# Kernel optimization log

Hardware: AMD Instinct MI355X
Metric: run time of the kernel (lower is better)

Reference implementation:

```python
import jax, jax.numpy as jnp
import numpy as np

EPS = 1e-12  # matches torch F.normalize default eps


def setup_inputs() -> dict:
    key = jax.random.key(0)
    k1, = jax.random.split(key, 1)
    N, M, D = 1024, 40, 768
    x = jax.random.normal(k1, (N, M, D), dtype=jnp.float32)
    w = jnp.asarray(15.0, dtype=jnp.float32)
    b = jnp.asarray(-7.0, dtype=jnp.float32)
    return {"x": x, "w": w, "b": b}


def reference(x, w, b):
    N, M, D = x.shape
    # L2 normalize along feature dim (torch F.normalize: x / max(||x||, eps))
    norm = jnp.linalg.norm(x, axis=-1, keepdims=True)
    xn = x / jnp.maximum(norm, EPS)
    # Inclusive centroids [N, D]
    c_incl = jnp.mean(xn, axis=1)
    # Exclusive centroids [N, M, D]: leave-one-out mean
    c_excl = (M * c_incl[:, None, :] - xn) / (M - 1)
    # Similarity of every utterance to every inclusive centroid: [N, M, N]
    sim = jnp.einsum('nmd,kd->nmk', xn, c_incl)
    # Own-speaker column uses the exclusive centroid instead (vectorized
    # replacement of the per-speaker diagonal-block loop)
    diag = jnp.sum(xn * c_excl, axis=-1)                 # [N, M]
    own = jnp.eye(N, dtype=bool)[:, None, :]             # [N, 1, N]
    sim = jnp.where(own, diag[:, :, None], sim)
    # Affine scale then cross-entropy against speaker labels
    logits = (w * sim + b).reshape(N * M, N)
    labels = jnp.repeat(jnp.arange(N), M)                # [N*M]
    lse = jax.nn.logsumexp(logits, axis=-1)
    picked = jnp.take_along_axis(logits, labels[:, None], axis=1)[:, 0]
    loss = jnp.mean(lse - picked)
    return loss
```

## Files before the change

kernel.cpp:

```cpp
#include <hip/hip_runtime.h>
#include <hip/hip_bf16.h>
#include <hip/hip_fp8.h>

typedef float f32x4 __attribute__((ext_vector_type(4)));
typedef long long i64;
typedef i64 i64x2 __attribute__((ext_vector_type(2)));

#define N_SPK 1024
#define M_UTT 40
#define D_FEAT 768
#define NROWS (N_SPK * M_UTT)
#define LOG2E 1.44269504088896340736f
#define LN2   0.69314718055994530942f

#define BM 128
#define BN 128
#define BKB 64
#define KT (D_FEAT / BKB)
#define ROWB 768

#define INV_SS (1.0f / 64.0f)
#define SCL 8.0f

__device__ __forceinline__ unsigned char to_fp8(float v) {
  __hip_fp8_e4m3 t(v);
  return (unsigned char)t.__x;
}

__device__ __forceinline__ int perm4base(int k0) {
  const int b = k0 & 63;
  return (k0 & ~63) + ((b >> 3) & 3) * 16 + (b & 7) + ((b >> 5) << 3);
}

__global__ __launch_bounds__(256) void k_norm_cent(const float* __restrict__ x,
                                                   unsigned char* __restrict__ xn,
                                                   unsigned char* __restrict__ cc) {
  const int n = blockIdx.x, t = threadIdx.x;
  const int lane = t & 63, wv = t >> 6;
  const float4* xb4 = (const float4*)(x + (size_t)n * (M_UTT * D_FEAT));
  unsigned char* ob = xn + (size_t)n * (M_UTT * D_FEAT);

  __shared__ float bins[2][4][3];
  __shared__ float cl[4][192][4];

  int o_[3], c4_[3], soff_[3];
#pragma unroll
  for (int q = 0; q < 3; ++q) {
    const int f = q * 256 + t;
    o_[q]  = f / 192;
    c4_[q] = f % 192;
    soff_[q] = perm4base(4 * c4_[q]);
  }

  float cacc[3][4];
#pragma unroll
  for (int q = 0; q < 3; ++q)
#pragma unroll
    for (int c = 0; c < 4; ++c) cacc[q][c] = 0.f;

  for (int g = 0; g < M_UTT / 4; ++g) {
    const int p = g & 1;
    float4 v[3];
#pragma unroll
    for (int q = 0; q < 3; ++q) v[q] = xb4[g * 768 + q * 256 + t];
    float ss[3];
#pragma unroll
    for (int q = 0; q < 3; ++q)
      ss[q] = v[q].x * v[q].x + v[q].y * v[q].y + v[q].z * v[q].z + v[q].w * v[q].w;
#pragma unroll
    for (int d = 1; d < 64; d <<= 1) {
      ss[0] += __shfl_xor(ss[0], d, 64);
      ss[1] += __shfl_xor(ss[1], d, 64);
      ss[2] += __shfl_xor(ss[2], d, 64);
    }
    if (lane == 0) {
#pragma unroll
      for (int q = 0; q < 3; ++q) {
        const int idx = 4 * q + wv;
        bins[p][idx / 3][idx % 3] = ss[q];
      }
    }
    __syncthreads();
#pragma unroll
    for (int q = 0; q < 3; ++q) {
      const int o = o_[q];
      const float tot = bins[p][o][0] + bins[p][o][1] + bins[p][o][2];
      const float iv = 1.0f / fmaxf(sqrtf(tot), 1e-12f);
      const float w0 = v[q].x * iv, w1 = v[q].y * iv, w2 = v[q].z * iv, w3 = v[q].w * iv;
      cacc[q][0] += w0; cacc[q][1] += w1; cacc[q][2] += w2; cacc[q][3] += w3;
      uchar4 u;
      u.x = to_fp8(w0 * SCL); u.y = to_fp8(w1 * SCL);
      u.z = to_fp8(w2 * SCL); u.w = to_fp8(w3 * SCL);
      *(uchar4*)(ob + (size_t)(4 * g + o) * D_FEAT + soff_[q]) = u;
    }
  }

#pragma unroll
  for (int q = 0; q < 3; ++q) {
#pragma unroll
    for (int c = 0; c < 4; ++c) cl[o_[q]][c4_[q]][c] = cacc[q][c];
  }
  __syncthreads();
  if (t < 192) {
    float s[4];
#pragma unroll
    for (int c = 0; c < 4; ++c)
      s[c] = cl[0][t][c] + cl[1][t][c] + cl[2][t][c] + cl[3][t][c];
    const float sc = SCL / (float)M_UTT;
    uchar4 u;
    u.x = to_fp8(s[0] * sc); u.y = to_fp8(s[1] * sc);
    u.z = to_fp8(s[2] * sc); u.w = to_fp8(s[3] * sc);
    *(uchar4*)(cc + (size_t)n * D_FEAT + perm4base(4 * t)) = u;
  }
}

#define GLD(g, l) __builtin_amdgcn_global_load_lds( \
    (const __attribute__((address_space(1))) unsigned int*)(g), \
    (__attribute__((address_space(3))) unsigned int*)(l), 16, 0, 0)

__global__ __launch_bounds__(256, 4) void k_gemm_part(
    const unsigned char* __restrict__ XN, const unsigned char* __restrict__ CC,
    const float* __restrict__ wp, const float* __restrict__ bp,
    float2* __restrict__ ppart, float* __restrict__ picked2) {

  __shared__ __align__(16) char smem[32768];

  const int tid  = threadIdx.x;
  const int wave = tid >> 6, lane = tid & 63;
  const int l16  = lane & 15, lg = lane >> 4;
  const int wr   = wave >> 1, wc = wave & 1;

  const int bid = blockIdx.x;
  const int xcd = bid & 7;
  const int tt  = bid >> 3;
  const int rb  = xcd * 40 + (tt >> 3);
  const int cb  = tt & 7;
  const int rowbase = rb * BM;
  const int colbase = cb * BN;

  const int R7   = (tid >> 3) & 7;
  const int li   = ((tid & 7) * 16) ^ (R7 << 4);
  const int row0 = 2 * (tid >> 3) + (li >> 6);
  const int kb   = li & 63;
  const int t16  = tid * 16;
  const unsigned char* gA = XN + (size_t)(rowbase + row0) * ROWB + kb;
  const unsigned char* gB = CC + (size_t)(colbase + row0) * ROWB + kb;

  const int xr  = ((l16 >> 1) & 7) << 4;
  const int in0 = ((((l16 & 1) << 6) | (lg << 4)) ^ xr);
  int aoff[4], boff[4];
#pragma unroll
  for (int i = 0; i < 4; ++i) {
    aoff[i] = (wr * 32 + i * 8 + (l16 >> 1)) * 128 + in0;
    boff[i] = 8192 + (wc * 32 + i * 8 + (l16 >> 1)) * 128 + in0;
  }

  f32x4 acc[4][4];
#pragma unroll
  for (int i = 0; i < 4; ++i)
#pragma unroll
    for (int jj = 0; jj < 4; ++jj) acc[i][jj] = (f32x4){0.f, 0.f, 0.f, 0.f};

  auto STAGE = [&](int buf, int koff) {
    char* sb = smem + buf * 16384;
    GLD(gA + koff,              sb + t16);
    GLD(gA + 64 * ROWB + koff,  sb + 4096 + t16);
    GLD(gB + koff,              sb + 8192 + t16);
    GLD(gB + 64 * ROWB + koff,  sb + 12288 + t16);
  };

  STAGE(0, 0);

  for (int k = 0; k < KT; ++k) {
    const char* bb = smem + (k & 1) * 16384;
    if (k + 1 < KT) {
      STAGE((k + 1) & 1, (k + 1) * BKB);
      asm volatile("s_waitcnt vmcnt(4)" ::: "memory");
    } else {
      asm volatile("s_waitcnt vmcnt(0)" ::: "memory");
    }
    __builtin_amdgcn_s_barrier();

    i64x2 av[4], bv[4];
#pragma unroll
    for (int i = 0; i < 4; ++i) av[i] = *(const i64x2*)(bb + aoff[i]);
#pragma unroll
    for (int jj = 0; jj < 4; ++jj) bv[jj] = *(const i64x2*)(bb + boff[jj]);
    __builtin_amdgcn_s_setprio(1);
#pragma unroll
    for (int i = 0; i < 4; ++i)
#pragma unroll
      for (int jj = 0; jj < 4; ++jj)
        acc[i][jj] = __builtin_amdgcn_mfma_f32_16x16x32_fp8_fp8(av[i][0], bv[jj][0], acc[i][jj], 0, 0, 0);
#pragma unroll
    for (int i = 0; i < 4; ++i)
#pragma unroll
      for (int jj = 0; jj < 4; ++jj)
        acc[i][jj] = __builtin_amdgcn_mfma_f32_16x16x32_fp8_fp8(av[i][1], bv[jj][1], acc[i][jj], 0, 0, 0);
    __builtin_amdgcn_s_setprio(0);
    asm volatile("s_waitcnt lgkmcnt(0)" ::: "memory");
    __builtin_amdgcn_s_barrier();
  }

  const float ws2 = wp[0] * LOG2E;
  const float b2  = bp[0] * LOG2E;
  float2* red = (float2*)smem;

#pragma unroll
  for (int i = 0; i < 4; ++i) {
#pragma unroll
    for (int rr = 0; rr < 4; ++rr) {
      const int lrow = wr * 64 + i * 16 + lg * 4 + rr;
      const int R = rowbase + lrow;
      const int n = R / M_UTT;
      float l2[4];
#pragma unroll
      for (int jj = 0; jj < 4; ++jj) {
        float sim = acc[i][jj][rr] * INV_SS;
        const int gc = colbase + wc * 64 + jj * 16 + l16;
        if (gc == n) {
          sim = (40.f * sim - 1.f) * (1.f / 39.f);
          picked2[R] = fmaf(ws2, sim, b2);
        }
        l2[jj] = fmaf(ws2, sim, b2);
      }
      float mx = fmaxf(fmaxf(l2[0], l2[1]), fmaxf(l2[2], l2[3]));
#pragma unroll
      for (int d = 1; d < 16; d <<= 1) mx = fmaxf(mx, __shfl_xor(mx, d, 64));
      float s = exp2f(l2[0] - mx) + exp2f(l2[1] - mx) +
                exp2f(l2[2] - mx) + exp2f(l2[3] - mx);
#pragma unroll
      for (int d = 1; d < 16; d <<= 1) s += __shfl_xor(s, d, 64);
      if (l16 == 0) red[lrow * 2 + wc] = make_float2(mx, s);
    }
  }
  __syncthreads();
  if (tid < 128) {
    const float2 p0 = red[tid * 2 + 0];
    const float2 p1 = red[tid * 2 + 1];
    const float m2 = fmaxf(p0.x, p1.x);
    const float ss = p0.y * exp2f(p0.x - m2) + p1.y * exp2f(p1.x - m2);
    ppart[(size_t)(rowbase + tid) * 8 + cb] = make_float2(m2, ss);
  }
}

__global__ __launch_bounds__(256) void k_combine(const float2* __restrict__ pp,
                                                 const float* __restrict__ picked2,
                                                 double* __restrict__ partial) {
  const int t = threadIdx.x;
  const int R = blockIdx.x * 256 + t;
  const float2* p = pp + (size_t)R * 8;
  float2 v[8];
#pragma unroll
  for (int j = 0; j < 8; ++j) v[j] = p[j];
  float m2 = v[0].x;
#pragma unroll
  for (int j = 1; j < 8; ++j) m2 = fmaxf(m2, v[j].x);
  float s = 0.f;
#pragma unroll
  for (int j = 0; j < 8; ++j) s += v[j].y * exp2f(v[j].x - m2);
  const float lse2 = m2 + log2f(s);
  const float rl = (lse2 - picked2[R]) * LN2;

  __shared__ double sm[256];
  sm[t] = (double)rl;
  __syncthreads();
  for (int off = 128; off > 0; off >>= 1) {
    if (t < off) sm[t] += sm[t + off];
    __syncthreads();
  }
  if (t == 0) partial[blockIdx.x] = sm[0];
}

__global__ __launch_bounds__(256) void k_reduce(const double* __restrict__ partial,
                                                float* __restrict__ out) {
  const int t = threadIdx.x;
  __shared__ double sm[256];
  sm[t] = (t < NROWS / 256) ? partial[t] : 0.0;
  __syncthreads();
  for (int off = 128; off > 0; off >>= 1) {
    if (t < off) sm[t] += sm[t + off];
    __syncthreads();
  }
  if (t == 0) out[0] = (float)(sm[0] / (double)NROWS);
}

extern "C" void kernel_launch(void* const* d_in, const int* in_sizes, int n_in,
                              void* d_out, int out_size, void* d_ws, size_t ws_size,
                              hipStream_t stream) {
  const float* x = (const float*)d_in[0];
  const float* w = (const float*)d_in[1];
  const float* b = (const float*)d_in[2];
  char* ws = (char*)d_ws;
  size_t off = 0;
  unsigned char* xn = (unsigned char*)(ws + off); off += (size_t)NROWS * D_FEAT;
  unsigned char* cc = (unsigned char*)(ws + off); off += (size_t)N_SPK * D_FEAT;
  off = (off + 255) & ~(size_t)255;
  float2* ppart   = (float2*)(ws + off); off += (size_t)NROWS * 8 * sizeof(float2);
  float* picked2  = (float*)(ws + off);  off += (size_t)NROWS * sizeof(float);
  off = (off + 255) & ~(size_t)255;
  double* partial = (double*)(ws + off); off += (size_t)(NROWS / 256) * sizeof(double);
  float* out = (float*)d_out;

  k_norm_cent<<<N_SPK, 256, 0, stream>>>(x, xn, cc);
  k_gemm_part<<<(NROWS / BM) * (N_SPK / BN), 256, 0, stream>>>(xn, cc, w, b, ppart, picked2);
  k_combine<<<NROWS / 256, 256, 0, stream>>>(ppart, picked2, partial);
  k_reduce<<<1, 256, 0, stream>>>(partial, out);
}
```

Before: 95.12 us.

## Enlarge GEMM row tile to 160 rows with a five-fragment MFMA loop

Raises the row tile of the fused similarity/logsumexp GEMM from 128 to 160. The grid becomes 2048 blocks, which gives a better wave count on the CUs and more reuse of each B tile across rows. A third async global-to-LDS load fills the extra 32 A rows, and threads that have nothing to load write into a dummy scratch region. The inner loop now loads each A fragment right before its MFMAs instead of preloading all of them. The cost is more accumulator registers (80) and more LDS per block, which may limit occupancy. The host launch must also change to match the new block count.

```diff
diff --git a/kernel.cpp b/kernel.cpp
--- a/kernel.cpp
+++ b/kernel.cpp
@@ -13,11 +13,15 @@
 #define LOG2E 1.44269504088896340736f
 #define LN2   0.69314718055994530942f
 
-#define BM 128
+#define BM 160
 #define BN 128
 #define BKB 64
 #define KT (D_FEAT / BKB)
 #define ROWB 768
+
+#define ABYTES 10240
+#define TILEB  18432
+#define SCRATCH 36864
 
 #define INV_SS (1.0f / 64.0f)
 #define SCL 8.0f
@@ -123,7 +127,7 @@
     const float* __restrict__ wp, const float* __restrict__ bp,
     float2* __restrict__ ppart, float* __restrict__ picked2) {
 
-  __shared__ __align__(16) char smem[32768];
+  __shared__ __align__(16) char smem[38912];
 
   const int tid  = threadIdx.x;
   const int wave = tid >> 6, lane = tid & 63;
@@ -132,71 +136,74 @@
 
   const int bid = blockIdx.x;
   const int xcd = bid & 7;
-  const int tt  = bid >> 3;
-  const int rb  = xcd * 40 + (tt >> 3);
-  const int cb  = tt & 7;
+  const int idx = bid >> 3;
+  const int rb  = xcd * 32 + (idx >> 3);
+  const int cb  = idx & 7;
   const int rowbase = rb * BM;
   const int colbase = cb * BN;
 
-  const int R7   = (tid >> 3) & 7;
-  const int li   = ((tid & 7) * 16) ^ (R7 << 4);
+  const int li   = ((tid & 7) * 16) ^ (((tid >> 3) & 7) << 4);
   const int row0 = 2 * (tid >> 3) + (li >> 6);
   const int kb   = li & 63;
   const int t16  = tid * 16;
   const unsigned char* gA = XN + (size_t)(rowbase + row0) * ROWB + kb;
   const unsigned char* gB = CC + (size_t)(colbase + row0) * ROWB + kb;
+  char* c2dst = (tid < 128) ? (char*)nullptr : nullptr;
 
   const int xr  = ((l16 >> 1) & 7) << 4;
   const int in0 = ((((l16 & 1) << 6) | (lg << 4)) ^ xr);
-  int aoff[4], boff[4];
-#pragma unroll
-  for (int i = 0; i < 4; ++i) {
-    aoff[i] = (wr * 32 + i * 8 + (l16 >> 1)) * 128 + in0;
-    boff[i] = 8192 + (wc * 32 + i * 8 + (l16 >> 1)) * 128 + in0;
-  }
-
-  f32x4 acc[4][4];
-#pragma unroll
-  for (int i = 0; i < 4; ++i)
+  int aoff[5], boff[4];
+#pragma unroll
+  for (int i = 0; i < 5; ++i)
+    aoff[i] = (wr * 40 + i * 8 + (l16 >> 1)) * 128 + in0;
+#pragma unroll
+  for (int jj = 0; jj < 4; ++jj)
+    boff[jj] = ABYTES + (wc * 32 + jj * 8 + (l16 >> 1)) * 128 + in0;
+
+  f32x4 acc[5][4];
+#pragma unroll
+  for (int i = 0; i < 5; ++i)
 #pragma unroll
     for (int jj = 0; jj < 4; ++jj) acc[i][jj] = (f32x4){0.f, 0.f, 0.f, 0.f};
 
   auto STAGE = [&](int buf, int koff) {
-    char* sb = smem + buf * 16384;
+    char* sb = smem + buf * TILEB;
     GLD(gA + koff,              sb + t16);
     GLD(gA + 64 * ROWB + koff,  sb + 4096 + t16);
-    GLD(gB + koff,              sb + 8192 + t16);
-    GLD(gB + 64 * ROWB + koff,  sb + 12288 + t16);
+    {
+      const unsigned char* src = (tid < 128) ? (gA + 128 * ROWB + koff) : (gA + koff);
+      char* dst = (tid < 128) ? (sb + 8192 + t16) : (smem + SCRATCH + (t16 - 2048));
+      GLD(src, dst);
+    }
+    GLD(gB + koff,              sb + ABYTES + t16);
+    GLD(gB + 64 * ROWB + koff,  sb + ABYTES + 4096 + t16);
   };
 
   STAGE(0, 0);
 
   for (int k = 0; k < KT; ++k) {
-    const char* bb = smem + (k & 1) * 16384;
+    const char* bb = smem + (k & 1) * TILEB;
     if (k + 1 < KT) {
       STAGE((k + 1) & 1, (k + 1) * BKB);
-      asm volatile("s_waitcnt vmcnt(4)" ::: "memory");
+      asm volatile("s_waitcnt vmcnt(5)" ::: "memory");
     } else {
       asm volatile("s_waitcnt vmcnt(0)" ::: "memory");
     }
     __builtin_amdgcn_s_barrier();
 
-    i64x2 av[4], bv[4];
-#pragma unroll
-    for (int i = 0; i < 4; ++i) av[i] = *(const i64x2*)(bb + aoff[i]);
+    i64x2 bv[4];
 #pragma unroll
     for (int jj = 0; jj < 4; ++jj) bv[jj] = *(const i64x2*)(bb + boff[jj]);
     __builtin_amdgcn_s_setprio(1);
 #pragma unroll
-    for (int i = 0; i < 4; ++i)
-#pragma unroll
-      for (int jj = 0; jj < 4; ++jj)
-        acc[i][jj] = __builtin_amdgcn_mfma_f32_16x16x32_fp8_fp8(av[i][0], bv[jj][0], acc[i][jj], 0, 0, 0);
-#pragma unroll
-    for (int i = 0; i < 4; ++i)
-#pragma unroll
-      for (int jj = 0; jj < 4; ++jj)
-        acc[i][jj] = __builtin_amdgcn_mfma_f32_16x16x32_fp8_fp8(av[i][1], bv[jj][1], acc[i][jj], 0, 0, 0);
+    for (int i = 0; i < 5; ++i) {
+      const i64x2 av = *(const i64x2*)(bb + aoff[i]);
+#pragma unroll
+      for (int jj = 0; jj < 4; ++jj) {
+        acc[i][jj] = __builtin_amdgcn_mfma_f32_16x16x32_fp8_fp8(av[0], bv[jj][0], acc[i][jj], 0, 0, 0);
+        acc[i][jj] = __builtin_amdgcn_mfma_f32_16x16x32_fp8_fp8(av[1], bv[jj][1], acc[i][jj], 0, 0, 0);
+      }
+    }
     __builtin_amdgcn_s_setprio(0);
     asm volatile("s_waitcnt lgkmcnt(0)" ::: "memory");
     __builtin_amdgcn_s_barrier();
@@ -207,10 +214,10 @@
   float2* red = (float2*)smem;
 
 #pragma unroll
-  for (int i = 0; i < 4; ++i) {
+  for (int i = 0; i < 5; ++i) {
 #pragma unroll
     for (int rr = 0; rr < 4; ++rr) {
-      const int lrow = wr * 64 + i * 16 + lg * 4 + rr;
+      const int lrow = wr * 80 + i * 16 + lg * 4 + rr;
       const int R = rowbase + lrow;
       const int n = R / M_UTT;
       float l2[4];
@@ -235,7 +242,7 @@
     }
   }
   __syncthreads();
-  if (tid < 128) {
+  if (tid < 160) {
     const float2 p0 = red[tid * 2 + 0];
     const float2 p1 = red[tid * 2 + 1];
     const float m2 = fmaxf(p0.x, p1.x);
```

Measured after the change: 108.8 us. 1.14x slower.
